# Kernel tuning notes

Hardware: AMD Instinct MI355X
Metric: run time of the kernel (lower is better)

## Reference

```python
import jax, jax.numpy as jnp
import numpy as np

# Inner-product factors for Cl(1,3) (Minkowski metric diag(+,-,-,-)).
# For blade e_b, <~e_b e_b>_0 = product of the metric signs of its constituent vectors.
# Blade order: [1, e0,e1,e2,e3, e01,e02,e03,e12,e13,e23, e012,e013,e023,e123, e0123]
_IPF = jnp.array([1, 1, -1, -1, -1, -1, -1, -1, 1, 1, 1, 1, 1, 1, -1, -1], dtype=jnp.float32)

B, H, N, CMV, CS = 4, 8, 2048, 8, 16


def setup_inputs() -> dict:
    key = jax.random.key(0)
    ks = jax.random.split(key, 6)
    f = lambda k, s: jax.random.normal(k, s, dtype=jnp.float32)
    return {
        "q_mv": f(ks[0], (B, H, N, CMV, 16)),
        "k_mv": f(ks[1], (B, H, N, CMV, 16)),
        "v_mv": f(ks[2], (B, H, N, CMV, 16)),
        "q_s": f(ks[3], (B, H, N, CS)),
        "k_s": f(ks[4], (B, H, N, CS)),
        "v_s": f(ks[5], (B, H, N, CS)),
    }


def reference(q_mv, k_mv, v_mv, q_s, k_s, v_s):
    b, h, n, cmv, _ = q_mv.shape
    cs = q_s.shape[-1]
    cmv_out = v_mv.shape[-2]
    cs_out = v_s.shape[-1]
    # GA inner product on mv part = euclidean dot after applying metric factors to queries
    q = jnp.concatenate([(q_mv * _IPF).reshape(b, h, n, cmv * 16), q_s], axis=-1)
    k = jnp.concatenate([k_mv.reshape(b, h, n, cmv * 16), k_s], axis=-1)
    v = jnp.concatenate([v_mv.reshape(b, h, n, cmv_out * 16), v_s], axis=-1)
    scale = 1.0 / np.sqrt(q.shape[-1]).astype(np.float32)  # torch SDPA default scale
    scores = jnp.einsum("bhid,bhjd->bhij", q, k) * scale  # [B,H,N,N]
    attn = jax.nn.softmax(scores, axis=-1)
    out = jnp.einsum("bhij,bhjd->bhid", attn, v)
    out_mv = out[..., : cmv_out * 16].reshape(b, h, n, cmv_out, 16)
    out_s = out[..., cmv_out * 16 : cmv_out * 16 + cs_out]
    return out_mv, out_s
```

## Files before the change

### kernel.cpp

```cpp
#include <hip/hip_runtime.h>
#include <cstdint>
#include <math.h>


#define BH    32
#define N_    2048
#define DMV   128
#define DS    16
#define D_    144
#define BM    128
#define BN    64
#define NKIT  (N_ / BN)
#define KSTR  152
#define VSTR  72
#define SVROWS 160
#define KCHUNKS (BN * KSTR / 8)
#define VCHUNKS (D_ * VSTR / 8)
#define KP_BYTES ((size_t)BH * N_ * KSTR * 2)
#define QSCALE 0.12022458674074693f
#define KPACK_BLOCKS (BH * N_ * 19 / 256)

typedef __bf16 bf16_8 __attribute__((ext_vector_type(8)));
typedef float  f32x4  __attribute__((ext_vector_type(4)));
typedef float  f32x16 __attribute__((ext_vector_type(16)));

#define GLOAD_LDS16(g, l)                                                     \
  __builtin_amdgcn_global_load_lds(                                           \
      (const __attribute__((address_space(1))) void*)(g),                     \
      (__attribute__((address_space(3))) void*)(l), 16, 0, 0)

__device__ __forceinline__ f32x16 mfma32(bf16_8 a, bf16_8 b, f32x16 c) {
  return __builtin_amdgcn_mfma_f32_32x32x16_bf16(a, b, c, 0, 0, 0);
}

__global__ __launch_bounds__(256)
void pack_kv(const float* __restrict__ kmv, const float* __restrict__ ks_,
             const float* __restrict__ vmv, const float* __restrict__ vs,
             __bf16* __restrict__ kp, __bf16* __restrict__ vt) {
  __shared__ __align__(16) __bf16 sT[D_ * VSTR];
  const int t = threadIdx.x;
  const int b = blockIdx.x;
  if (b < KPACK_BLOCKS) {
    const unsigned g = b * 256u + t;
    const unsigned row = g / 19u, seg = g - row * 19u;
    bf16_8 o;
    if (seg < 16) {
      const f32x4* p = (const f32x4*)(kmv + (size_t)row * DMV + seg * 8);
      f32x4 a = p[0], bb = p[1];
#pragma unroll
      for (int j = 0; j < 8; ++j) o[j] = (__bf16)((j < 4) ? a[j] : bb[j - 4]);
    } else if (seg < 18) {
      const f32x4* p = (const f32x4*)(ks_ + (size_t)row * DS + (seg - 16) * 8);
      f32x4 a = p[0], bb = p[1];
#pragma unroll
      for (int j = 0; j < 8; ++j) o[j] = (__bf16)((j < 4) ? a[j] : bb[j - 4]);
    } else {
#pragma unroll
      for (int j = 0; j < 8; ++j) o[j] = (__bf16)0.0f;
    }
    *(bf16_8*)(kp + (size_t)row * KSTR + seg * 8) = o;
    return;
  }
  const int tile = b - KPACK_BLOCKS;
  const int n = t >> 2, c = t & 3;
  const float* mv = vmv + (size_t)(tile * 64 + n) * DMV;
  const float* sv = vs  + (size_t)(tile * 64 + n) * DS;
  if (c < 3) {
#pragma unroll
    for (int i = 0; i < 9; ++i) {
      f32x4 q = *(const f32x4*)(mv + c * 36 + 4 * i);
#pragma unroll
      for (int j = 0; j < 4; ++j) sT[(c * 36 + 4 * i + j) * VSTR + n] = (__bf16)q[j];
    }
  } else {
#pragma unroll
    for (int i = 0; i < 5; ++i) {
      f32x4 q = *(const f32x4*)(mv + 108 + 4 * i);
#pragma unroll
      for (int j = 0; j < 4; ++j) sT[(108 + 4 * i + j) * VSTR + n] = (__bf16)q[j];
    }
#pragma unroll
    for (int i = 0; i < 4; ++i) {
      f32x4 q = *(const f32x4*)(sv + 4 * i);
#pragma unroll
      for (int j = 0; j < 4; ++j) sT[(DMV + 4 * i + j) * VSTR + n] = (__bf16)q[j];
    }
  }
  __syncthreads();
  __bf16* vtt = vt + (size_t)tile * (D_ * VSTR);
#pragma unroll
  for (int s = 0; s < 5; ++s) {
    int idx = t + 256 * s;
    if (idx < D_ * 8) {
      int d = idx >> 3, jc = idx & 7;
      *(bf16_8*)&vtt[d * VSTR + jc * 8] = *(const bf16_8*)&sT[d * VSTR + jc * 8];
    }
  }
}

__device__ __forceinline__ bf16_8 load_q_frag(const float* qmv_row, const float* qs_row, int k0) {
  bf16_8 f;
  if (k0 < DMV) {
    const f32x4* p = (const f32x4*)(qmv_row + k0);
    f32x4 a = p[0], b = p[1];
    int hi8 = k0 & 8;
#pragma unroll
    for (int j = 0; j < 8; ++j) {
      float v = (j < 4) ? a[j] : b[j - 4];
      bool pos = hi8 ? (j < 6) : (j < 2);
      f[j] = (__bf16)(v * (pos ? QSCALE : -QSCALE));
    }
  } else {
    const f32x4* p = (const f32x4*)(qs_row + (k0 - DMV));
    f32x4 a = p[0], b = p[1];
#pragma unroll
    for (int j = 0; j < 8; ++j) {
      float v = (j < 4) ? a[j] : b[j - 4];
      f[j] = (__bf16)(v * QSCALE);
    }
  }
  return f;
}

__global__ __launch_bounds__(256, 2)
void geo_attn_kernel(const float* __restrict__ q_mv, const float* __restrict__ q_s,
                     const __bf16* __restrict__ kp, const __bf16* __restrict__ vt,
                     float* __restrict__ out)
{
  __shared__ __align__(16) __bf16 sK[BN * KSTR];
  __shared__ __align__(16) __bf16 sVT[SVROWS * VSTR];

  const int tid  = threadIdx.x;
  const int w    = tid >> 6;
  const int lane = tid & 63;
  const int c32  = lane & 31;
  const int hi   = lane >> 5;
  const int bh    = blockIdx.y;
  const int qbase = blockIdx.x * BM;
  const size_t bh_n = (size_t)bh * N_;

  if (tid < 144) {
    f32x4 z = {0.f, 0.f, 0.f, 0.f};
    *(f32x4*)((char*)sVT + D_ * VSTR * 2 + tid * 16) = z;
  }

  bf16_8 qf[9];
  {
    const int mrow = qbase + w * 32 + c32;
    const float* qmv_row = q_mv + (bh_n + mrow) * DMV;
    const float* qs_row  = q_s  + (bh_n + mrow) * DS;
#pragma unroll
    for (int ks = 0; ks < 9; ++ks)
      qf[ks] = load_q_frag(qmv_row, qs_row, ks * 16 + hi * 8);
  }

  f32x16 of[5];
#pragma unroll
  for (int dt = 0; dt < 5; ++dt)
#pragma unroll
    for (int r = 0; r < 16; ++r) of[dt][r] = 0.0f;
  float m_i = -INFINITY, l_i = 0.0f;

  const __bf16* kbase = kp + bh_n * KSTR;

  for (int it = 0; it < NKIT; ++it) {
    {
      const __bf16* kt  = kbase + (size_t)(it * BN) * KSTR;
      const __bf16* vtt = vt + (size_t)(bh * NKIT + it) * (D_ * VSTR);
#pragma unroll
      for (int s = 0; s < 4; ++s)
        GLOAD_LDS16(kt + (tid + 256 * s) * 8, &sK[(tid + 256 * s) * 8]);
      if (tid < KCHUNKS - 1024)
        GLOAD_LDS16(kt + (tid + 1024) * 8, &sK[(tid + 1024) * 8]);
#pragma unroll
      for (int s = 0; s < 5; ++s)
        GLOAD_LDS16(vtt + (tid + 256 * s) * 8, &sVT[(tid + 256 * s) * 8]);
      if (tid < VCHUNKS - 1280)
        GLOAD_LDS16(vtt + (tid + 1280) * 8, &sVT[(tid + 1280) * 8]);
    }
    __syncthreads();

    f32x16 sf[2];
#pragma unroll
    for (int nt = 0; nt < 2; ++nt)
#pragma unroll
      for (int r = 0; r < 16; ++r) sf[nt][r] = 0.0f;
    __builtin_amdgcn_s_setprio(1);
#pragma unroll
    for (int ks = 0; ks < 9; ++ks) {
      bf16_8 kb0 = *(const bf16_8*)&sK[(c32)      * KSTR + ks * 16 + hi * 8];
      bf16_8 kb1 = *(const bf16_8*)&sK[(32 + c32) * KSTR + ks * 16 + hi * 8];
      sf[0] = mfma32(kb0, qf[ks], sf[0]);
      sf[1] = mfma32(kb1, qf[ks], sf[1]);
    }
    __builtin_amdgcn_s_setprio(0);

    float al = 1.0f, m_use;
    {
      float mx = sf[0][0];
#pragma unroll
      for (int r = 1; r < 16; ++r) mx = fmaxf(mx, sf[0][r]);
#pragma unroll
      for (int r = 0; r < 16; ++r) mx = fmaxf(mx, sf[1][r]);
      mx = fmaxf(mx, __shfl_xor(mx, 32));

      if (__all(mx <= m_i + 8.0f)) {
        m_use = m_i;
      } else {
        float mnew = fmaxf(m_i, mx);
        al = __builtin_amdgcn_exp2f(m_i - mnew);
        m_i = mnew; m_use = mnew;
#pragma unroll
        for (int r = 0; r < 16; ++r) {
          float a = __shfl(al, (r & 3) + 8 * (r >> 2) + 4 * hi);
#pragma unroll
          for (int dt = 0; dt < 5; ++dt) of[dt][r] *= a;
        }
      }
      float rs = 0.0f;
#pragma unroll
      for (int nt = 0; nt < 2; ++nt)
#pragma unroll
        for (int r = 0; r < 16; ++r) {
          float p = __builtin_amdgcn_exp2f(sf[nt][r] - m_use);
          sf[nt][r] = p;
          rs += p;
        }
      rs += __shfl_xor(rs, 32);
      l_i = l_i * al + rs;
    }

#pragma unroll
    for (int ks = 0; ks < 4; ++ks) {
      const int nt = ks >> 1;
      const int Ra = 8 * (ks & 1);
      unsigned x0, x1, y0, y1;
      asm("v_cvt_pk_bf16_f32 %0, %1, %2" : "=v"(x0) : "v"(sf[nt][Ra + 0]), "v"(sf[nt][Ra + 1]));
      asm("v_cvt_pk_bf16_f32 %0, %1, %2" : "=v"(x1) : "v"(sf[nt][Ra + 2]), "v"(sf[nt][Ra + 3]));
      asm("v_cvt_pk_bf16_f32 %0, %1, %2" : "=v"(y0) : "v"(sf[nt][Ra + 4]), "v"(sf[nt][Ra + 5]));
      asm("v_cvt_pk_bf16_f32 %0, %1, %2" : "=v"(y1) : "v"(sf[nt][Ra + 6]), "v"(sf[nt][Ra + 7]));
      auto s0 = __builtin_amdgcn_permlane32_swap(x0, y0, false, false);
      auto s1 = __builtin_amdgcn_permlane32_swap(x1, y1, false, false);
      union { unsigned u[4]; bf16_8 v; } pu;
      pu.u[0] = s0[0]; pu.u[1] = s1[0]; pu.u[2] = s0[1]; pu.u[3] = s1[1];
      __builtin_amdgcn_s_setprio(1);
#pragma unroll
      for (int dt = 0; dt < 5; ++dt) {
        bf16_8 vb = *(const bf16_8*)&sVT[(dt * 32 + c32) * VSTR + ks * 16 + hi * 8];
        of[dt] = mfma32(pu.v, vb, of[dt]);
      }
      __builtin_amdgcn_s_setprio(0);
    }
    __syncthreads();
  }

  float* out_mv = out;
  float* out_s  = out + (size_t)BH * N_ * DMV;
#pragma unroll
  for (int r = 0; r < 16; ++r) {
    const int ml  = (r & 3) + 8 * (r >> 2) + 4 * hi;
    const float linv = __builtin_amdgcn_rcpf(__shfl(l_i, ml));
    const int row = qbase + w * 32 + ml;
#pragma unroll
    for (int dt = 0; dt < 4; ++dt)
      out_mv[(bh_n + row) * DMV + dt * 32 + c32] = of[dt][r] * linv;
    if (c32 < DS)
      out_s[(bh_n + row) * DS + c32] = of[4][r] * linv;
  }
}

extern "C" void kernel_launch(void* const* d_in, const int* in_sizes, int n_in,
                              void* d_out, int out_size, void* d_ws, size_t ws_size,
                              hipStream_t stream) {
  (void)in_sizes; (void)n_in; (void)out_size; (void)ws_size;
  const float* q_mv = (const float*)d_in[0];
  const float* k_mv = (const float*)d_in[1];
  const float* v_mv = (const float*)d_in[2];
  const float* q_s  = (const float*)d_in[3];
  const float* k_s  = (const float*)d_in[4];
  const float* v_s  = (const float*)d_in[5];
  float* out = (float*)d_out;

  __bf16* kp = (__bf16*)d_ws;
  __bf16* vt = (__bf16*)((char*)d_ws + KP_BYTES);

  pack_kv<<<KPACK_BLOCKS + BH * NKIT, 256, 0, stream>>>(k_mv, k_s, v_mv, v_s, kp, vt);

  dim3 grid(N_ / BM, BH);
  geo_attn_kernel<<<grid, 256, 0, stream>>>(q_mv, q_s, kp, vt, out);
}
```

Measured before the change: 244.0 us.

## Double-buffer K/V tiles, widen to 512-thread blocks, XCD-aware grid, rework V transpose

The attention kernel now uses 512 threads covering 256 query rows per block, which halves how often each K/V tile is loaded per query. K/V tiles are double-buffered in LDS so the next tile's global-to-LDS loads are issued while the current tile is being computed. The grid is flattened and remapped so that blocks sharing a head land on the same XCD, which should improve L2 reuse. The pack kernel's V transpose writes row-major into LDS and reads it back transposed in pairs. Together these roughly double LDS use per block, and with launch bounds of (512, 2) they raise register pressure and may lower occupancy.

```diff
diff --git a/kernel.cpp b/kernel.cpp
--- a/kernel.cpp
+++ b/kernel.cpp
@@ -8,7 +8,7 @@
 #define DMV   128
 #define DS    16
 #define D_    144
-#define BM    128
+#define BM    256
 #define BN    64
 #define NKIT  (N_ / BN)
 #define KSTR  152
@@ -19,8 +19,11 @@
 #define KP_BYTES ((size_t)BH * N_ * KSTR * 2)
 #define QSCALE 0.12022458674074693f
 #define KPACK_BLOCKS (BH * N_ * 19 / 256)
+#define TSTR  156
 
 typedef __bf16 bf16_8 __attribute__((ext_vector_type(8)));
+typedef __bf16 bf16_4 __attribute__((ext_vector_type(4)));
+typedef __bf16 bf16_2 __attribute__((ext_vector_type(2)));
 typedef float  f32x4  __attribute__((ext_vector_type(4)));
 typedef float  f32x16 __attribute__((ext_vector_type(16)));
 
@@ -33,11 +36,16 @@
   return __builtin_amdgcn_mfma_f32_32x32x16_bf16(a, b, c, 0, 0, 0);
 }
 
+__device__ __forceinline__ bf16_4 cvt4(f32x4 x) {
+  bf16_4 w; w[0]=(__bf16)x[0]; w[1]=(__bf16)x[1]; w[2]=(__bf16)x[2]; w[3]=(__bf16)x[3];
+  return w;
+}
+
 __global__ __launch_bounds__(256)
 void pack_kv(const float* __restrict__ kmv, const float* __restrict__ ks_,
              const float* __restrict__ vmv, const float* __restrict__ vs,
              __bf16* __restrict__ kp, __bf16* __restrict__ vt) {
-  __shared__ __align__(16) __bf16 sT[D_ * VSTR];
+  __shared__ __align__(16) __bf16 sT[64 * TSTR];
   const int t = threadIdx.x;
   const int b = blockIdx.x;
   if (b < KPACK_BLOCKS) {
@@ -65,36 +73,27 @@
   const int n = t >> 2, c = t & 3;
   const float* mv = vmv + (size_t)(tile * 64 + n) * DMV;
   const float* sv = vs  + (size_t)(tile * 64 + n) * DS;
+  __bf16* row = &sT[n * TSTR];
   if (c < 3) {
 #pragma unroll
-    for (int i = 0; i < 9; ++i) {
-      f32x4 q = *(const f32x4*)(mv + c * 36 + 4 * i);
-#pragma unroll
-      for (int j = 0; j < 4; ++j) sT[(c * 36 + 4 * i + j) * VSTR + n] = (__bf16)q[j];
-    }
+    for (int i = 0; i < 9; ++i)
+      *(bf16_4*)&row[c * 36 + 4 * i] = cvt4(*(const f32x4*)(mv + c * 36 + 4 * i));
   } else {
 #pragma unroll
-    for (int i = 0; i < 5; ++i) {
-      f32x4 q = *(const f32x4*)(mv + 108 + 4 * i);
-#pragma unroll
-      for (int j = 0; j < 4; ++j) sT[(108 + 4 * i + j) * VSTR + n] = (__bf16)q[j];
-    }
-#pragma unroll
-    for (int i = 0; i < 4; ++i) {
-      f32x4 q = *(const f32x4*)(sv + 4 * i);
-#pragma unroll
-      for (int j = 0; j < 4; ++j) sT[(DMV + 4 * i + j) * VSTR + n] = (__bf16)q[j];
-    }
+    for (int i = 0; i < 5; ++i)
+      *(bf16_4*)&row[108 + 4 * i] = cvt4(*(const f32x4*)(mv + 108 + 4 * i));
+#pragma unroll
+    for (int i = 0; i < 4; ++i)
+      *(bf16_4*)&row[128 + 4 * i] = cvt4(*(const f32x4*)(sv + 4 * i));
   }
   __syncthreads();
   __bf16* vtt = vt + (size_t)tile * (D_ * VSTR);
 #pragma unroll
-  for (int s = 0; s < 5; ++s) {
-    int idx = t + 256 * s;
-    if (idx < D_ * 8) {
-      int d = idx >> 3, jc = idx & 7;
-      *(bf16_8*)&vtt[d * VSTR + jc * 8] = *(const bf16_8*)&sT[d * VSTR + jc * 8];
-    }
+  for (int k = 0; k < 18; ++k) {
+    int idx = t + 256 * k;
+    int d = idx >> 5, j = idx & 31;
+    bf16_2 p; p[0] = sT[(2 * j) * TSTR + d]; p[1] = sT[(2 * j + 1) * TSTR + d];
+    *(bf16_2*)&vtt[d * VSTR + 2 * j] = p;
   }
 }
 
@@ -122,26 +121,31 @@
   return f;
 }
 
-__global__ __launch_bounds__(256, 2)
+__global__ __launch_bounds__(512, 2)
 void geo_attn_kernel(const float* __restrict__ q_mv, const float* __restrict__ q_s,
                      const __bf16* __restrict__ kp, const __bf16* __restrict__ vt,
                      float* __restrict__ out)
 {
-  __shared__ __align__(16) __bf16 sK[BN * KSTR];
-  __shared__ __align__(16) __bf16 sVT[SVROWS * VSTR];
+  __shared__ __align__(16) __bf16 sK[2][BN * KSTR];
+  __shared__ __align__(16) __bf16 sVT[2][SVROWS * VSTR];
 
   const int tid  = threadIdx.x;
   const int w    = tid >> 6;
   const int lane = tid & 63;
   const int c32  = lane & 31;
   const int hi   = lane >> 5;
-  const int bh    = blockIdx.y;
-  const int qbase = blockIdx.x * BM;
+  const int flat = blockIdx.x;
+  const int xcd  = flat & 7;
+  const int jj   = flat >> 3;
+  const int bh   = xcd * 4 + (jj & 3);
+  const int qb   = jj >> 2;
+  const int qbase = qb * BM;
   const size_t bh_n = (size_t)bh * N_;
 
-  if (tid < 144) {
+  if (tid < 288) {
+    int bb = tid / 144, cc = tid - bb * 144;
     f32x4 z = {0.f, 0.f, 0.f, 0.f};
-    *(f32x4*)((char*)sVT + D_ * VSTR * 2 + tid * 16) = z;
+    *(f32x4*)((char*)&sVT[bb][D_ * VSTR] + cc * 16) = z;
   }
 
   bf16_8 qf[9];
@@ -162,23 +166,31 @@
   float m_i = -INFINITY, l_i = 0.0f;
 
   const __bf16* kbase = kp + bh_n * KSTR;
+  const __bf16* vbase = vt + (size_t)bh * NKIT * (D_ * VSTR);
+
+  auto stage = [&](int it, int bu) {
+    const __bf16* kt  = kbase + (size_t)(it * BN) * KSTR;
+    const __bf16* vtt = vbase + (size_t)it * (D_ * VSTR);
+    __bf16* dK = &sK[bu][0];
+    __bf16* dV = &sVT[bu][0];
+#pragma unroll
+    for (int s = 0; s < 2; ++s)
+      GLOAD_LDS16(kt + (tid + 512 * s) * 8, dK + (tid + 512 * s) * 8);
+    if (tid < KCHUNKS - 1024)
+      GLOAD_LDS16(kt + (tid + 1024) * 8, dK + (tid + 1024) * 8);
+#pragma unroll
+    for (int s = 0; s < 2; ++s)
+      GLOAD_LDS16(vtt + (tid + 512 * s) * 8, dV + (tid + 512 * s) * 8);
+    if (tid < VCHUNKS - 1024)
+      GLOAD_LDS16(vtt + (tid + 1024) * 8, dV + (tid + 1024) * 8);
+  };
+
+  stage(0, 0);
+  __syncthreads();
 
   for (int it = 0; it < NKIT; ++it) {
-    {
-      const __bf16* kt  = kbase + (size_t)(it * BN) * KSTR;
-      const __bf16* vtt = vt + (size_t)(bh * NKIT + it) * (D_ * VSTR);
-#pragma unroll
-      for (int s = 0; s < 4; ++s)
-        GLOAD_LDS16(kt + (tid + 256 * s) * 8, &sK[(tid + 256 * s) * 8]);
-      if (tid < KCHUNKS - 1024)
-        GLOAD_LDS16(kt + (tid + 1024) * 8, &sK[(tid + 1024) * 8]);
-#pragma unroll
-      for (int s = 0; s < 5; ++s)
-        GLOAD_LDS16(vtt + (tid + 256 * s) * 8, &sVT[(tid + 256 * s) * 8]);
-      if (tid < VCHUNKS - 1280)
-        GLOAD_LDS16(vtt + (tid + 1280) * 8, &sVT[(tid + 1280) * 8]);
-    }
-    __syncthreads();
+    const int cur = it & 1;
+    if (it + 1 < NKIT) stage(it + 1, cur ^ 1);
 
     f32x16 sf[2];
 #pragma unroll
@@ -188,8 +200,8 @@
     __builtin_amdgcn_s_setprio(1);
 #pragma unroll
     for (int ks = 0; ks < 9; ++ks) {
-      bf16_8 kb0 = *(const bf16_8*)&sK[(c32)      * KSTR + ks * 16 + hi * 8];
-      bf16_8 kb1 = *(const bf16_8*)&sK[(32 + c32) * KSTR + ks * 16 + hi * 8];
+      bf16_8 kb0 = *(const bf16_8*)&sK[cur][(c32)      * KSTR + ks * 16 + hi * 8];
+      bf16_8 kb1 = *(const bf16_8*)&sK[cur][(32 + c32) * KSTR + ks * 16 + hi * 8];
       sf[0] = mfma32(kb0, qf[ks], sf[0]);
       sf[1] = mfma32(kb1, qf[ks], sf[1]);
     }
@@ -246,7 +258,7 @@
       __builtin_amdgcn_s_setprio(1);
 #pragma unroll
       for (int dt = 0; dt < 5; ++dt) {
-        bf16_8 vb = *(const bf16_8*)&sVT[(dt * 32 + c32) * VSTR + ks * 16 + hi * 8];
+        bf16_8 vb = *(const bf16_8*)&sVT[cur][(dt * 32 + c32) * VSTR + ks * 16 + hi * 8];
         of[dt] = mfma32(pu.v, vb, of[dt]);
       }
       __builtin_amdgcn_s_setprio(0);
@@ -286,6 +298,5 @@
 
   pack_kv<<<KPACK_BLOCKS + BH * NKIT, 256, 0, stream>>>(k_mv, k_s, v_mv, v_s, kp, vt);
 
-  dim3 grid(N_ / BM, BH);
-  geo_attn_kernel<<<grid, 256, 0, stream>>>(q_mv, q_s, kp, vt, out);
-}
+  geo_attn_kernel<<<dim3(256), 512, 0, stream>>>(q_mv, q_s, kp, vt, out);
+}
```

Result: no change. 239.5 us (-1.9%).
